# Kernel optimization log

Measured on AMD Instinct MI355X. Metric: run time of the kernel, lower is better.

## Reference

```python
import jax, jax.numpy as jnp
import numpy as np

D_VISION = 1024
D_BRANCH = 256
N_BRANCHES = 4
N_HEADS = 4
HEAD_DIM = D_BRANCH // N_HEADS
DIVERSITY_WEIGHT = 0.1
LN_EPS = 1e-5


def setup_inputs() -> dict:
    key = jax.random.key(0)
    ks = jax.random.split(key, 8)
    B, T, N = 8, 16, 256
    frame_patches = jax.random.normal(ks[0], (B, T, N, D_VISION), dtype=jnp.float32)
    # LayerNorm params (shared input_norm)
    ln_gamma = jnp.ones((D_VISION,), jnp.float32)
    ln_beta = jnp.zeros((D_VISION,), jnp.float32)
    # Per-branch params stacked on a leading branch dim
    query = jax.random.normal(ks[1], (N_BRANCHES, N_HEADS, HEAD_DIM), jnp.float32) * 0.02
    wstd = 1.0 / np.sqrt(D_VISION)
    Wk = jax.random.uniform(ks[2], (N_BRANCHES, D_VISION, D_BRANCH), jnp.float32, -wstd, wstd)
    bk = jax.random.uniform(ks[3], (N_BRANCHES, D_BRANCH), jnp.float32, -wstd, wstd)
    Wv = jax.random.uniform(ks[4], (N_BRANCHES, D_VISION, D_BRANCH), jnp.float32, -wstd, wstd)
    bv = jax.random.uniform(ks[5], (N_BRANCHES, D_BRANCH), jnp.float32, -wstd, wstd)
    ostd = 1.0 / np.sqrt(D_BRANCH)
    Wo = jax.random.uniform(ks[6], (N_BRANCHES, D_BRANCH, D_BRANCH), jnp.float32, -ostd, ostd)
    bo = jax.random.uniform(ks[7], (N_BRANCHES, D_BRANCH), jnp.float32, -ostd, ostd)
    return dict(frame_patches=frame_patches, ln_gamma=ln_gamma, ln_beta=ln_beta,
                query=query, Wk=Wk, bk=bk, Wv=Wv, bv=bv, Wo=Wo, bo=bo)


def _layernorm(x, g, b):
    mu = jnp.mean(x, axis=-1, keepdims=True)
    var = jnp.var(x, axis=-1, keepdims=True)
    return (x - mu) * jax.lax.rsqrt(var + LN_EPS) * g + b


def reference(frame_patches, ln_gamma, ln_beta, query, Wk, bk, Wv, bv, Wo, bo):
    B, T, N, D = frame_patches.shape
    nb, H, hd = query.shape
    db = H * hd
    scale = hd ** -0.5
    x = _layernorm(frame_patches.reshape(B * T, N, D), ln_gamma, ln_beta)  # (BT, N, D)
    # Batched k/v projections across all branches (the fusion opportunity)
    k = (jnp.einsum('bpd,ndk->nbpk', x, Wk) + bk[:, None, None, :]).reshape(nb, B * T, N, H, hd)
    v = (jnp.einsum('bpd,ndk->nbpk', x, Wv) + bv[:, None, None, :]).reshape(nb, B * T, N, H, hd)
    # Single learnable query per (branch, head) attends over patches
    scores = jnp.einsum('nbphd,nhd->nbhp', k, query) * scale  # (nb, BT, H, N)
    attn = jax.nn.softmax(scores, axis=-1)
    attn_avg = attn.mean(axis=2)  # (nb, BT, N) head-averaged, pre-dropout
    # Dropout is inference no-op (eval mode)
    pooled = jnp.einsum('nbhp,nbphd->nbhd', attn, v).reshape(nb, B * T, db)
    out = jnp.einsum('nbk,nkj->nbj', pooled, Wo) + bo[:, None, :]  # (nb, BT, db)
    streams = out.transpose(1, 0, 2).reshape(B, T, nb, db)
    # Diversity loss: mean pairwise cosine similarity of attention distributions
    norms = jnp.maximum(jnp.linalg.norm(attn_avg, axis=-1, keepdims=True), 1e-8)
    a = attn_avg / norms
    sims = jnp.einsum('ibn,jbn->ijb', a, a).mean(axis=-1)  # (nb, nb)
    mask = jnp.triu(jnp.ones((nb, nb), attn_avg.dtype), k=1)
    diversity_loss = DIVERSITY_WEIGHT * (sims * mask).sum() / mask.sum()
    return streams, diversity_loss
```

## Files before the change

### kernel.cpp

```cpp
#include <hip/hip_runtime.h>
#include <stdint.h>

#define BT      128
#define NPATCH  256
#define DV      1024
#define NB      4
#define DB      256
#define NH16    16
#define SCALE   0.125f
#define LNEPS   1e-5f

#define OFF_BWS    16384u
#define OFF_PSC    24608u
#define OFF_DRAW   25120u
#define OFF_STATS  549408u
#define OFF_CV     1139232u
#define OFF_DIV    1141280u
#define OFF_XBAR   1142048u
#define OFF_POOL   9530656u
#define XSLICE     2097152u

#define LROW 264

typedef short bf16x8 __attribute__((ext_vector_type(8)));
typedef float f32x4  __attribute__((ext_vector_type(4)));

__device__ __forceinline__ short f2bf(float f) {
    union { float f; unsigned u; } v; v.f = f;
    unsigned u = v.u;
    unsigned r = (u + 0x7fffu + ((u >> 16) & 1u)) >> 16;
    return (short)r;
}

__device__ __forceinline__ unsigned pk2(float lo, float hi) {
    union { float f; unsigned u; } a, b; a.f = lo; b.f = hi;
    return __builtin_amdgcn_perm(b.u, a.u, 0x07060302u);
}

__global__ __launch_bounds__(256) void kP(const float* __restrict__ Wk,
                                          const float* __restrict__ q,
                                          const float* __restrict__ g,
                                          const float* __restrict__ b,
                                          float* __restrict__ ws) {
    const int nh = blockIdx.x >> 4, ich = blockIdx.x & 15;
    const int n = nh >> 2, h = nh & 3;
    __shared__ float qs[64];
    __shared__ float redS[4], redC[4];
    const int t = threadIdx.x;
    if (t < 64) qs[t] = q[nh * 64 + t];
    __syncthreads();
    const int r = t >> 2, qd = t & 3;
    const int i = ich * 64 + r;
    const float* wrow = Wk + ((size_t)n * DV + i) * DB + h * 64 + qd * 16;
    float acc = 0.f;
    #pragma unroll
    for (int d = 0; d < 16; d += 4) {
        float4 w4 = *(const float4*)(wrow + d);
        acc += w4.x * qs[qd * 16 + d]     + w4.y * qs[qd * 16 + d + 1]
             + w4.z * qs[qd * 16 + d + 2] + w4.w * qs[qd * 16 + d + 3];
    }
    acc += __shfl_xor(acc, 1);
    acc += __shfl_xor(acc, 2);
    float gw = g[i] * acc;
    if (qd == 0) {
        unsigned short* bws = (unsigned short*)(ws + OFF_BWS);
        const int kt = i >> 5, oct = (r >> 3) & 3, j = r & 7;
        bws[((kt * 64 + oct * 16 + nh) << 3) + j] = (unsigned short)f2bf(gw);
    }
    float mS = (qd == 0) ? gw : 0.f;
    float mC = (qd == 0) ? b[i] * acc : 0.f;
    #pragma unroll
    for (int dd = 4; dd < 64; dd <<= 1) { mS += __shfl_xor(mS, dd); mC += __shfl_xor(mC, dd); }
    const int wave = t >> 6, lane = t & 63;
    if (lane == 0) { redS[wave] = mS; redC[wave] = mC; }
    __syncthreads();
    if (t == 0) {
        ws[OFF_PSC + (nh * 16 + ich) * 2 + 0] = redS[0] + redS[1] + redS[2] + redS[3];
        ws[OFF_PSC + (nh * 16 + ich) * 2 + 1] = redC[0] + redC[1] + redC[2] + redC[3];
    }
}

__global__ __launch_bounds__(256) void kA(const float* __restrict__ x,
                                          float* __restrict__ ws) {
    __shared__ unsigned short xs[64 * LROW];
    const int t = threadIdx.x;
    const int wv = t >> 6, lane = t & 63;
    const int m = lane & 15, oct = lane >> 4;
    const int row0 = blockIdx.x * 64;
    const bf16x8* bfp = (const bf16x8*)((const unsigned short*)(ws + OFF_BWS));
    const float* xb = x + (size_t)row0 * DV;

    float sum[16], sq[16];
    #pragma unroll
    for (int i = 0; i < 16; ++i) { sum[i] = 0.f; sq[i] = 0.f; }
    f32x4 acc = {0.f, 0.f, 0.f, 0.f};
    float4 r[16];

    auto loadr = [&](int c) {
        #pragma unroll
        for (int i = 0; i < 16; ++i)
            r[i] = *(const float4*)(xb + (size_t)(i * 4 + wv) * DV + c * 256 + lane * 4);
    };
    auto commit = [&]() {
        #pragma unroll
        for (int i = 0; i < 16; ++i) {
            float4 v = r[i];
            sum[i] += v.x + v.y + v.z + v.w;
            sq[i]  += v.x * v.x + v.y * v.y + v.z * v.z + v.w * v.w;
            uint2 pk; pk.x = pk2(v.x, v.y); pk.y = pk2(v.z, v.w);
            *(uint2*)&xs[(i * 4 + wv) * LROW + lane * 4] = pk;
        }
    };
    auto comp = [&](int c) {
        #pragma unroll
        for (int kt = 0; kt < 8; ++kt) {
            bf16x8 af = *(const bf16x8*)&xs[(wv * 16 + m) * LROW + kt * 32 + oct * 8];
            bf16x8 bf = bfp[(c * 8 + kt) * 64 + lane];
            acc = __builtin_amdgcn_mfma_f32_16x16x32_bf16(af, bf, acc, 0, 0, 0);
        }
    };

    loadr(0);
    for (int c = 0; c < 4; ++c) {
        __syncthreads();
        commit();
        __syncthreads();
        if (c < 3) loadr(c + 1);
        comp(c);
    }

    #pragma unroll
    for (int r2 = 0; r2 < 4; ++r2)
        ws[OFF_DRAW + (size_t)(row0 + wv * 16 + oct * 4 + r2) * 16 + m] = acc[r2];

    #pragma unroll
    for (int i = 0; i < 16; ++i) {
        float s = sum[i], q2 = sq[i];
        #pragma unroll
        for (int d = 1; d < 64; d <<= 1) { s += __shfl_xor(s, d); q2 += __shfl_xor(q2, d); }
        if (lane == 0) {
            const int row = row0 + i * 4 + wv;
            const float mu  = s * (1.f / 1024.f);
            const float var = q2 * (1.f / 1024.f) - mu * mu;
            float2 st; st.x = mu; st.y = rsqrtf(var + LNEPS);
            *(float2*)(ws + OFF_STATS + (size_t)row * 2) = st;
        }
    }
}

__global__ __launch_bounds__(256) void kC(const float* __restrict__ x,
                                          const float* __restrict__ q,
                                          const float* __restrict__ bk,
                                          float* __restrict__ ws) {
    const int bt = blockIdx.x;
    const int qq = blockIdx.y;
    const int t = threadIdx.x;
    __shared__ __attribute__((aligned(16))) float s_s[NH16 * NPATCH];
    __shared__ __attribute__((aligned(16))) float aavg[NB * NPATCH];
    __shared__ __attribute__((aligned(16))) float w_s[64 * 16];
    __shared__ __attribute__((aligned(16))) float rstd_s[NPATCH];
    __shared__ __attribute__((aligned(16))) float mrs[NPATCH];
    __shared__ float Ss[NH16], Cbs[NH16];

    {
        const int nh = t >> 4, ich = t & 15;
        float S = ws[OFF_PSC + t * 2 + 0];
        float C = ws[OFF_PSC + t * 2 + 1];
        const int n2 = nh >> 2, h2 = nh & 3;
        const float* bkp = bk + n2 * DB + h2 * 64 + ich * 4;
        const float* qp  = q + nh * 64 + ich * 4;
        C += bkp[0] * qp[0] + bkp[1] * qp[1] + bkp[2] * qp[2] + bkp[3] * qp[3];
        #pragma unroll
        for (int d = 1; d < 16; d <<= 1) { S += __shfl_xor(S, d); C += __shfl_xor(C, d); }
        if (ich == 0) { Ss[nh] = S; Cbs[nh] = C; }
    }
    const size_t row = (size_t)bt * NPATCH + t;
    const float2 st = *(const float2*)(ws + OFF_STATS + row * 2);
    rstd_s[t] = st.y;
    mrs[t] = st.x * st.y;
    __syncthreads();

    const float* dr = ws + OFF_DRAW + row * 16;
    #pragma unroll
    for (int nh = 0; nh < NH16; ++nh)
        s_s[nh * NPATCH + t] = (st.y * (dr[nh] - st.x * Ss[nh]) + Cbs[nh]) * SCALE;
    __syncthreads();

    const int wave = t >> 6, lane = t & 63;
    for (int r = 0; r < 4; ++r) {
        const int nh = wave * 4 + r;
        float4 v = *(float4*)&s_s[nh * NPATCH + lane * 4];
        float mx = fmaxf(fmaxf(v.x, v.y), fmaxf(v.z, v.w));
        for (int d = 1; d < 64; d <<= 1) mx = fmaxf(mx, __shfl_xor(mx, d));
        float e0 = __expf(v.x - mx), e1 = __expf(v.y - mx);
        float e2 = __expf(v.z - mx), e3 = __expf(v.w - mx);
        float s = e0 + e1 + e2 + e3;
        for (int d = 1; d < 64; d <<= 1) s += __shfl_xor(s, d);
        float inv = 1.f / s;
        float4 a; a.x = e0 * inv; a.y = e1 * inv; a.z = e2 * inv; a.w = e3 * inv;
        *(float4*)&s_s[nh * NPATCH + lane * 4] = a;
    }
    __syncthreads();

    if (qq == 0) {
        for (int r = 0; r < 4; ++r) {
            const int nh = wave * 4 + r;
            float4 a4 = *(float4*)&s_s[nh * NPATCH + lane * 4];
            float4 m4 = *(float4*)&mrs[lane * 4];
            float dd = a4.x * m4.x + a4.y * m4.y + a4.z * m4.z + a4.w * m4.w;
            for (int d = 1; d < 64; d <<= 1) dd += __shfl_xor(dd, d);
            if (lane == 0) ws[OFF_CV + bt * NH16 + nh] = dd;
        }
        #pragma unroll
        for (int nb2 = 0; nb2 < NB; ++nb2)
            aavg[nb2 * NPATCH + t] = 0.25f * (s_s[(nb2 * 4 + 0) * NPATCH + t] + s_s[(nb2 * 4 + 1) * NPATCH + t]
                                            + s_s[(nb2 * 4 + 2) * NPATCH + t] + s_s[(nb2 * 4 + 3) * NPATCH + t]);
        __syncthreads();
        if (wave == 0) {
            float nrm[NB];
            #pragma unroll
            for (int nb2 = 0; nb2 < NB; ++nb2) {
                float4 v = *(float4*)&aavg[nb2 * NPATCH + lane * 4];
                float ss = v.x * v.x + v.y * v.y + v.z * v.z + v.w * v.w;
                for (int d = 1; d < 64; d <<= 1) ss += __shfl_xor(ss, d);
                nrm[nb2] = fmaxf(sqrtf(ss), 1e-8f);
            }
            int pi = 0;
            for (int i2 = 0; i2 < NB; ++i2)
                for (int j2 = i2 + 1; j2 < NB; ++j2) {
                    float4 va = *(float4*)&aavg[i2 * NPATCH + lane * 4];
                    float4 vb = *(float4*)&aavg[j2 * NPATCH + lane * 4];
                    float dd = va.x * vb.x + va.y * vb.y + va.z * vb.z + va.w * vb.w;
                    for (int d = 1; d < 64; d <<= 1) dd += __shfl_xor(dd, d);
                    if (lane == 0) ws[OFF_DIV + bt * 6 + pi] = dd / (nrm[i2] * nrm[j2]);
                    ++pi;
                }
        }
    }

    for (int idx = t; idx < 1024; idx += 256) {
        const int p = idx >> 4, nh = idx & 15;
        w_s[idx] = s_s[nh * NPATCH + qq * 64 + p] * rstd_s[qq * 64 + p];
    }
    __syncthreads();

    float4 acc[16];
    #pragma unroll
    for (int i = 0; i < 16; ++i) { acc[i].x = 0.f; acc[i].y = 0.f; acc[i].z = 0.f; acc[i].w = 0.f; }
    const float* xp = x + (size_t)(bt * NPATCH + qq * 64) * DV + t * 4;
    #define FMA4(k, wgt, xv) acc[k].x += (wgt) * xv.x; acc[k].y += (wgt) * xv.y; \
                             acc[k].z += (wgt) * xv.z; acc[k].w += (wgt) * xv.w;
    #define PBLOCK(p, xv) { \
        float4 a0 = *(const float4*)&w_s[(p) * 16 + 0]; \
        float4 a1 = *(const float4*)&w_s[(p) * 16 + 4]; \
        float4 a2 = *(const float4*)&w_s[(p) * 16 + 8]; \
        float4 a3 = *(const float4*)&w_s[(p) * 16 + 12]; \
        FMA4(0, a0.x, xv)  FMA4(1, a0.y, xv)  FMA4(2, a0.z, xv)  FMA4(3, a0.w, xv) \
        FMA4(4, a1.x, xv)  FMA4(5, a1.y, xv)  FMA4(6, a1.z, xv)  FMA4(7, a1.w, xv) \
        FMA4(8, a2.x, xv)  FMA4(9, a2.y, xv)  FMA4(10, a2.z, xv) FMA4(11, a2.w, xv) \
        FMA4(12, a3.x, xv) FMA4(13, a3.y, xv) FMA4(14, a3.z, xv) FMA4(15, a3.w, xv) }
    for (int p = 0; p < 16; ++p) {
        float4 xv0 = *(const float4*)(xp + (size_t)(p +  0) * DV);
        float4 xv1 = *(const float4*)(xp + (size_t)(p + 16) * DV);
        float4 xv2 = *(const float4*)(xp + (size_t)(p + 32) * DV);
        float4 xv3 = *(const float4*)(xp + (size_t)(p + 48) * DV);
        PBLOCK(p, xv0)
        PBLOCK(p + 16, xv1)
        PBLOCK(p + 32, xv2)
        PBLOCK(p + 48, xv3)
    }
    #undef PBLOCK
    #undef FMA4
    unsigned short* xb16 = (unsigned short*)(ws + OFF_XBAR);
    #pragma unroll
    for (int nh = 0; nh < 16; ++nh) {
        float4 a = acc[nh];
        uint2 pk;
        pk.x = (unsigned)(unsigned short)f2bf(a.x) | ((unsigned)(unsigned short)f2bf(a.y) << 16);
        pk.y = (unsigned)(unsigned short)f2bf(a.z) | ((unsigned)(unsigned short)f2bf(a.w) << 16);
        *(uint2*)&xb16[(size_t)qq * XSLICE + ((size_t)bt * NH16 + nh) * DV + t * 4] = pk;
    }
}

__global__ __launch_bounds__(256) void kD1(const float* __restrict__ Wv,
                                           const float* __restrict__ g,
                                           const float* __restrict__ b,
                                           const float* __restrict__ bv,
                                           float* __restrict__ ws) {
    const int nh = blockIdx.x & 15, btg = blockIdx.x >> 4;
    const int n = nh >> 2, h = nh & 3;
    const int bt0 = btg * 4, cb = h * 64;
    __shared__ __attribute__((aligned(16))) float xs[4][1024];
    __shared__ __attribute__((aligned(16))) float gs[1024], bs[1024];
    __shared__ float red[4][64][6];
    const int t = threadIdx.x;
    const unsigned short* xb16 = (const unsigned short*)(ws + OFF_XBAR);
    for (int e = t; e < 1024; e += 256) {
        const int bt = e >> 8, i4 = e & 255;
        const size_t b0 = ((size_t)(bt0 + bt) * NH16 + nh) * DV + i4 * 4;
        float sx = 0.f, sy = 0.f, sz = 0.f, sw = 0.f;
        #pragma unroll
        for (int qq = 0; qq < 4; ++qq) {
            uint2 pv = *(const uint2*)&xb16[b0 + (size_t)qq * XSLICE];
            union { unsigned u; float f; } c0, c1, c2, c3;
            c0.u = pv.x << 16; c1.u = pv.x & 0xffff0000u;
            c2.u = pv.y << 16; c3.u = pv.y & 0xffff0000u;
            sx += c0.f; sy += c1.f; sz += c2.f; sw += c3.f;
        }
        float4 s; s.x = sx; s.y = sy; s.z = sz; s.w = sw;
        *(float4*)&xs[bt][i4 * 4] = s;
    }
    for (int e = t; e < 1024; e += 256) { gs[e] = g[e]; bs[e] = b[e]; }
    __syncthreads();
    const int c = t & 63, sub = t >> 6;
    float acc[4];
    #pragma unroll
    for (int l = 0; l < 4; ++l) acc[l] = 0.f;
    float gv = 0.f, bvv = 0.f;
    const float* wvp = Wv + ((size_t)n * DV + sub * 256) * DB + cb + c;
    const int ib0 = sub * 256;
    #pragma unroll 2
    for (int gidx = 0; gidx < 64; ++gidx) {
        const int ib = ib0 + gidx * 4;
        float w0 = wvp[(size_t)(gidx * 4 + 0) * DB];
        float w1 = wvp[(size_t)(gidx * 4 + 1) * DB];
        float w2 = wvp[(size_t)(gidx * 4 + 2) * DB];
        float w3 = wvp[(size_t)(gidx * 4 + 3) * DB];
        float4 g4 = *(const float4*)&gs[ib];
        float4 b4 = *(const float4*)&bs[ib];
        float q0 = g4.x * w0, q1 = g4.y * w1, q2 = g4.z * w2, q3 = g4.w * w3;
        gv  += q0 + q1 + q2 + q3;
        bvv += b4.x * w0 + b4.y * w1 + b4.z * w2 + b4.w * w3;
        #pragma unroll
        for (int l = 0; l < 4; ++l) {
            float4 xr = *(const float4*)&xs[l][ib];
            acc[l] += xr.x * q0 + xr.y * q1 + xr.z * q2 + xr.w * q3;
        }
    }
    #pragma unroll
    for (int l = 0; l < 4; ++l) red[sub][c][l] = acc[l];
    red[sub][c][4] = gv; red[sub][c][5] = bvv;
    __syncthreads();
    const int c2 = t & 63, l = t >> 6;
    float gvS = red[0][c2][4] + red[1][c2][4] + red[2][c2][4] + red[3][c2][4];
    float bvS = red[0][c2][5] + red[1][c2][5] + red[2][c2][5] + red[3][c2][5];
    float base = bv[n * DB + cb + c2] + bvS;
    float p = red[0][c2][l] + red[1][c2][l] + red[2][c2][l] + red[3][c2][l];
    float C = ws[OFF_CV + (bt0 + l) * NH16 + nh];
    ws[OFF_POOL + ((size_t)n * BT + bt0 + l) * DB + cb + c2] = p - C * gvS + base;
}

__global__ __launch_bounds__(256) void kD2(const float* __restrict__ Wo,
                                           const float* __restrict__ bo,
                                           const float* __restrict__ ws,
                                           float* __restrict__ out) {
    const int btg = blockIdx.x & 15, jq = (blockIdx.x >> 4) & 3, n = blockIdx.x >> 6;
    const int bt0 = btg * 8, j0 = jq * 64;
    __shared__ __attribute__((aligned(16))) float ps[8][256];
    __shared__ float red[4][64][8];
    __shared__ float dred[4];
    const int t = threadIdx.x;
    for (int e = t; e < 512; e += 256) {
        const int bt = e >> 6, c4 = e & 63;
        *(float4*)&ps[bt][c4 * 4] =
            *(const float4*)(ws + OFF_POOL + ((size_t)n * BT + bt0 + bt) * DB + c4 * 4);
    }
    float dacc = 0.f;
    if (blockIdx.x == 0)
        for (int idx = t; idx < 768; idx += 256) dacc += ws[OFF_DIV + idx];
    for (int d = 1; d < 64; d <<= 1) dacc += __shfl_xor(dacc, d);
    if ((t & 63) == 0) dred[t >> 6] = dacc;
    __syncthreads();
    if (blockIdx.x == 0 && t == 0)
        out[131072] = 0.1f * (dred[0] + dred[1] + dred[2] + dred[3]) / 768.f;
    const int j = t & 63, sub = t >> 6;
    float acc[8];
    #pragma unroll
    for (int l = 0; l < 8; ++l) acc[l] = 0.f;
    const float* wop = Wo + ((size_t)n * DB + sub * 64) * DB + j0 + j;
    const int cb0 = sub * 64;
    #pragma unroll 2
    for (int gidx = 0; gidx < 16; ++gidx) {
        const int cb = cb0 + gidx * 4;
        float w0 = wop[(size_t)(gidx * 4 + 0) * DB];
        float w1 = wop[(size_t)(gidx * 4 + 1) * DB];
        float w2 = wop[(size_t)(gidx * 4 + 2) * DB];
        float w3 = wop[(size_t)(gidx * 4 + 3) * DB];
        #pragma unroll
        for (int l = 0; l < 8; ++l) {
            float4 pr = *(const float4*)&ps[l][cb];
            acc[l] += pr.x * w0 + pr.y * w1 + pr.z * w2 + pr.w * w3;
        }
    }
    #pragma unroll
    for (int l = 0; l < 8; ++l) red[sub][j][l] = acc[l];
    __syncthreads();
    const int j2 = t & 63, l0 = t >> 6;
    float bov = bo[n * DB + j0 + j2];
    #pragma unroll
    for (int li = 0; li < 2; ++li) {
        const int l = l0 + li * 4;
        float o = red[0][j2][l] + red[1][j2][l] + red[2][j2][l] + red[3][j2][l] + bov;
        out[((size_t)(bt0 + l) * NB + n) * DB + j0 + j2] = o;
    }
}

extern "C" void kernel_launch(void* const* d_in, const int* in_sizes, int n_in,
                              void* d_out, int out_size, void* d_ws, size_t ws_size,
                              hipStream_t stream) {
    const float* x  = (const float*)d_in[0];
    const float* g  = (const float*)d_in[1];
    const float* b  = (const float*)d_in[2];
    const float* q  = (const float*)d_in[3];
    const float* Wk = (const float*)d_in[4];
    const float* bk = (const float*)d_in[5];
    const float* Wv = (const float*)d_in[6];
    const float* bv = (const float*)d_in[7];
    const float* Wo = (const float*)d_in[8];
    const float* bo = (const float*)d_in[9];
    float* out = (float*)d_out;
    float* ws  = (float*)d_ws;

    hipLaunchKernelGGL(kP,  dim3(256),    dim3(256), 0, stream, Wk, q, g, b, ws);
    hipLaunchKernelGGL(kA,  dim3(512),    dim3(256), 0, stream, x, ws);
    hipLaunchKernelGGL(kC,  dim3(128, 4), dim3(256), 0, stream, x, q, bk, ws);
    hipLaunchKernelGGL(kD1, dim3(512),    dim3(256), 0, stream, Wv, g, b, bv, ws);
    hipLaunchKernelGGL(kD2, dim3(256),    dim3(256), 0, stream, Wo, bo, ws, out);
}
```

Before: 278.3 us.

## Fuse V-projection pooling and output projection into one kernel

Merges kD1 (V projection of the attention-weighted patch sum) and kD2 (output projection) into a single 512-thread kernel. Each block handles one branch and two bt rows across all heads, keeping the pooled vector in shared memory instead of writing it to the workspace and reading it back. This removes one launch and the pooled round trip. In exchange each block streams a full branch slice of Wv and Wo for only two rows, so total weight reads rise, and the block grid shrinks from 512 to 256.

After: 321.7 us. 15.6% more time.

```diff
diff --git a/kernel.cpp b/kernel.cpp
--- a/kernel.cpp
+++ b/kernel.cpp
@@ -17,7 +17,6 @@
 #define OFF_CV     1139232u
 #define OFF_DIV    1141280u
 #define OFF_XBAR   1142048u
-#define OFF_POOL   9530656u
 #define XSLICE     2097152u
 
 #define LROW 264
@@ -282,21 +281,28 @@
     }
 }
 
-__global__ __launch_bounds__(256) void kD1(const float* __restrict__ Wv,
-                                           const float* __restrict__ g,
-                                           const float* __restrict__ b,
-                                           const float* __restrict__ bv,
-                                           float* __restrict__ ws) {
-    const int nh = blockIdx.x & 15, btg = blockIdx.x >> 4;
-    const int n = nh >> 2, h = nh & 3;
-    const int bt0 = btg * 4, cb = h * 64;
-    __shared__ __attribute__((aligned(16))) float xs[4][1024];
+__global__ __launch_bounds__(512) void kD(const float* __restrict__ Wv,
+                                          const float* __restrict__ Wo,
+                                          const float* __restrict__ g,
+                                          const float* __restrict__ b,
+                                          const float* __restrict__ bv,
+                                          const float* __restrict__ bo,
+                                          const float* __restrict__ ws,
+                                          float* __restrict__ out) {
+    const int n = blockIdx.x >> 6, btg = blockIdx.x & 63;
+    const int bt0 = btg * 2;
+    __shared__ __attribute__((aligned(16))) float zs[2][4][1024];
     __shared__ __attribute__((aligned(16))) float gs[1024], bs[1024];
-    __shared__ float red[4][64][6];
+    __shared__ __attribute__((aligned(16))) float red[2][256][4];
+    __shared__ __attribute__((aligned(16))) float pooled[2][256];
+    __shared__ float dred[8];
     const int t = threadIdx.x;
     const unsigned short* xb16 = (const unsigned short*)(ws + OFF_XBAR);
-    for (int e = t; e < 1024; e += 256) {
-        const int bt = e >> 8, i4 = e & 255;
+
+    for (int e = t; e < 2048; e += 512) {
+        const int bt = e >> 10, rem = e & 1023;
+        const int h = rem >> 8, i4 = rem & 255;
+        const int nh = n * 4 + h;
         const size_t b0 = ((size_t)(bt0 + bt) * NH16 + nh) * DV + i4 * 4;
         float sx = 0.f, sy = 0.f, sz = 0.f, sw = 0.f;
         #pragma unroll
@@ -308,100 +314,74 @@
             sx += c0.f; sy += c1.f; sz += c2.f; sw += c3.f;
         }
         float4 s; s.x = sx; s.y = sy; s.z = sz; s.w = sw;
-        *(float4*)&xs[bt][i4 * 4] = s;
-    }
-    for (int e = t; e < 1024; e += 256) { gs[e] = g[e]; bs[e] = b[e]; }
-    __syncthreads();
-    const int c = t & 63, sub = t >> 6;
-    float acc[4];
-    #pragma unroll
-    for (int l = 0; l < 4; ++l) acc[l] = 0.f;
-    float gv = 0.f, bvv = 0.f;
-    const float* wvp = Wv + ((size_t)n * DV + sub * 256) * DB + cb + c;
-    const int ib0 = sub * 256;
-    #pragma unroll 2
-    for (int gidx = 0; gidx < 64; ++gidx) {
-        const int ib = ib0 + gidx * 4;
-        float w0 = wvp[(size_t)(gidx * 4 + 0) * DB];
-        float w1 = wvp[(size_t)(gidx * 4 + 1) * DB];
-        float w2 = wvp[(size_t)(gidx * 4 + 2) * DB];
-        float w3 = wvp[(size_t)(gidx * 4 + 3) * DB];
-        float4 g4 = *(const float4*)&gs[ib];
-        float4 b4 = *(const float4*)&bs[ib];
-        float q0 = g4.x * w0, q1 = g4.y * w1, q2 = g4.z * w2, q3 = g4.w * w3;
-        gv  += q0 + q1 + q2 + q3;
-        bvv += b4.x * w0 + b4.y * w1 + b4.z * w2 + b4.w * w3;
-        #pragma unroll
-        for (int l = 0; l < 4; ++l) {
-            float4 xr = *(const float4*)&xs[l][ib];
-            acc[l] += xr.x * q0 + xr.y * q1 + xr.z * q2 + xr.w * q3;
-        }
-    }
-    #pragma unroll
-    for (int l = 0; l < 4; ++l) red[sub][c][l] = acc[l];
-    red[sub][c][4] = gv; red[sub][c][5] = bvv;
-    __syncthreads();
-    const int c2 = t & 63, l = t >> 6;
-    float gvS = red[0][c2][4] + red[1][c2][4] + red[2][c2][4] + red[3][c2][4];
-    float bvS = red[0][c2][5] + red[1][c2][5] + red[2][c2][5] + red[3][c2][5];
-    float base = bv[n * DB + cb + c2] + bvS;
-    float p = red[0][c2][l] + red[1][c2][l] + red[2][c2][l] + red[3][c2][l];
-    float C = ws[OFF_CV + (bt0 + l) * NH16 + nh];
-    ws[OFF_POOL + ((size_t)n * BT + bt0 + l) * DB + cb + c2] = p - C * gvS + base;
-}
-
-__global__ __launch_bounds__(256) void kD2(const float* __restrict__ Wo,
-                                           const float* __restrict__ bo,
-                                           const float* __restrict__ ws,
-                                           float* __restrict__ out) {
-    const int btg = blockIdx.x & 15, jq = (blockIdx.x >> 4) & 3, n = blockIdx.x >> 6;
-    const int bt0 = btg * 8, j0 = jq * 64;
-    __shared__ __attribute__((aligned(16))) float ps[8][256];
-    __shared__ float red[4][64][8];
-    __shared__ float dred[4];
-    const int t = threadIdx.x;
-    for (int e = t; e < 512; e += 256) {
-        const int bt = e >> 6, c4 = e & 63;
-        *(float4*)&ps[bt][c4 * 4] =
-            *(const float4*)(ws + OFF_POOL + ((size_t)n * BT + bt0 + bt) * DB + c4 * 4);
+        *(float4*)&zs[bt][h][i4 * 4] = s;
+    }
+    for (int e = t; e < 1024; e += 512) { gs[e] = g[e]; bs[e] = b[e]; }
+    __syncthreads();
+
+    const int c = t & 255, half = t >> 8, h = c >> 6, nh = n * 4 + h;
+    {
+        float a0 = 0.f, a1 = 0.f, gv = 0.f, bvv = 0.f;
+        const float* wvp = Wv + ((size_t)n * DV + half * 512) * DB + c;
+        const float* z0 = &zs[0][h][half * 512];
+        const float* z1 = &zs[1][h][half * 512];
+        const float* gp = &gs[half * 512];
+        const float* bp = &bs[half * 512];
+        #pragma unroll 4
+        for (int i = 0; i < 512; ++i) {
+            float w  = wvp[(size_t)i * DB];
+            float gw = gp[i] * w;
+            gv  += gw;
+            bvv += bp[i] * w;
+            a0  += z0[i] * gw;
+            a1  += z1[i] * gw;
+        }
+        red[half][c][0] = a0; red[half][c][1] = a1;
+        red[half][c][2] = gv; red[half][c][3] = bvv;
     }
     float dacc = 0.f;
-    if (blockIdx.x == 0)
-        for (int idx = t; idx < 768; idx += 256) dacc += ws[OFF_DIV + idx];
+    if (blockIdx.x == 0 && half == 1)
+        for (int idx = c; idx < 768; idx += 256) dacc += ws[OFF_DIV + idx];
+    #pragma unroll
     for (int d = 1; d < 64; d <<= 1) dacc += __shfl_xor(dacc, d);
     if ((t & 63) == 0) dred[t >> 6] = dacc;
     __syncthreads();
+
+    if (half == 0) {
+        float A0 = red[0][c][0] + red[1][c][0];
+        float A1 = red[0][c][1] + red[1][c][1];
+        float GV = red[0][c][2] + red[1][c][2];
+        float BV = red[0][c][3] + red[1][c][3];
+        float base = bv[n * DB + c] + BV;
+        float C0 = ws[OFF_CV + (bt0 + 0) * NH16 + nh];
+        float C1 = ws[OFF_CV + (bt0 + 1) * NH16 + nh];
+        pooled[0][c] = A0 - C0 * GV + base;
+        pooled[1][c] = A1 - C1 * GV + base;
+    }
     if (blockIdx.x == 0 && t == 0)
-        out[131072] = 0.1f * (dred[0] + dred[1] + dred[2] + dred[3]) / 768.f;
-    const int j = t & 63, sub = t >> 6;
-    float acc[8];
-    #pragma unroll
-    for (int l = 0; l < 8; ++l) acc[l] = 0.f;
-    const float* wop = Wo + ((size_t)n * DB + sub * 64) * DB + j0 + j;
-    const int cb0 = sub * 64;
-    #pragma unroll 2
-    for (int gidx = 0; gidx < 16; ++gidx) {
-        const int cb = cb0 + gidx * 4;
-        float w0 = wop[(size_t)(gidx * 4 + 0) * DB];
-        float w1 = wop[(size_t)(gidx * 4 + 1) * DB];
-        float w2 = wop[(size_t)(gidx * 4 + 2) * DB];
-        float w3 = wop[(size_t)(gidx * 4 + 3) * DB];
-        #pragma unroll
-        for (int l = 0; l < 8; ++l) {
-            float4 pr = *(const float4*)&ps[l][cb];
-            acc[l] += pr.x * w0 + pr.y * w1 + pr.z * w2 + pr.w * w3;
-        }
-    }
-    #pragma unroll
-    for (int l = 0; l < 8; ++l) red[sub][j][l] = acc[l];
-    __syncthreads();
-    const int j2 = t & 63, l0 = t >> 6;
-    float bov = bo[n * DB + j0 + j2];
-    #pragma unroll
-    for (int li = 0; li < 2; ++li) {
-        const int l = l0 + li * 4;
-        float o = red[0][j2][l] + red[1][j2][l] + red[2][j2][l] + red[3][j2][l] + bov;
-        out[((size_t)(bt0 + l) * NB + n) * DB + j0 + j2] = o;
+        out[131072] = 0.1f * (dred[4] + dred[5] + dred[6] + dred[7]) / 768.f;
+    __syncthreads();
+
+    {
+        float o0 = 0.f, o1 = 0.f;
+        const float* wop = Wo + ((size_t)n * DB + half * 128) * DB + c;
+        const float* p0 = &pooled[0][half * 128];
+        const float* p1 = &pooled[1][half * 128];
+        #pragma unroll 4
+        for (int cc = 0; cc < 128; ++cc) {
+            float w = wop[(size_t)cc * DB];
+            o0 += p0[cc] * w;
+            o1 += p1[cc] * w;
+        }
+        red[half][c][0] = o0; red[half][c][1] = o1;
+    }
+    __syncthreads();
+    if (half == 0) {
+        float bov = bo[n * DB + c];
+        float O0 = red[0][c][0] + red[1][c][0] + bov;
+        float O1 = red[0][c][1] + red[1][c][1] + bov;
+        out[((size_t)(bt0 + 0) * NB + n) * DB + c] = O0;
+        out[((size_t)(bt0 + 1) * NB + n) * DB + c] = O1;
     }
 }
 
@@ -421,9 +401,8 @@
     float* out = (float*)d_out;
     float* ws  = (float*)d_ws;
 
-    hipLaunchKernelGGL(kP,  dim3(256),    dim3(256), 0, stream, Wk, q, g, b, ws);
-    hipLaunchKernelGGL(kA,  dim3(512),    dim3(256), 0, stream, x, ws);
-    hipLaunchKernelGGL(kC,  dim3(128, 4), dim3(256), 0, stream, x, q, bk, ws);
-    hipLaunchKernelGGL(kD1, dim3(512),    dim3(256), 0, stream, Wv, g, b, bv, ws);
-    hipLaunchKernelGGL(kD2, dim3(256),    dim3(256), 0, stream, Wo, bo, ws, out);
-}
+    hipLaunchKernelGGL(kP, dim3(256),    dim3(256), 0, stream, Wk, q, g, b, ws);
+    hipLaunchKernelGGL(kA, dim3(512),    dim3(256), 0, stream, x, ws);
+    hipLaunchKernelGGL(kC, dim3(128, 4), dim3(256), 0, stream, x, q, bk, ws);
+    hipLaunchKernelGGL(kD, dim3(256),    dim3(512), 0, stream, Wv, Wo, g, b, bv, bo, ws, out);
+}
```
